# Kernel optimization log

Measured on AMD Instinct MI355X. Metric: run time of the kernel, lower is better.

The kernel has to match this reference:

```python
import jax, jax.numpy as jnp
import numpy as np

B, ES, HS, NL, NOUT, T = 16384, 64, 64, 3, 2, 128


def setup_inputs() -> dict:
    key = jax.random.key(0)
    ks = jax.random.split(key, 9)
    k = 1.0 / np.sqrt(HS)
    u = lambda kk, shape: jax.random.uniform(kk, shape, jnp.float32, -k, k)
    return {
        "agentFutureTrajEnc": jax.random.normal(ks[0], (B, ES), jnp.float32),
        "emb_w": u(ks[1], (ES, ES)),
        "emb_b": u(ks[2], (ES,)),
        "w_ih": u(ks[3], (NL, 3 * HS, ES)),
        "w_hh": u(ks[4], (NL, 3 * HS, HS)),
        "b_ih": u(ks[5], (NL, 3 * HS)),
        "b_hh": u(ks[6], (NL, 3 * HS)),
        "out_w": u(ks[7], (NOUT, HS)),
        "out_b": u(ks[8], (NOUT,)),
        "target_length": T,
        "batch_size": B,
    }


def _gru_cell(x, h, Wi, Wh, bi, bh):
    # PyTorch GRU cell math: gates ordered (r, z, n)
    gi = x @ Wi.T + bi            # (B, 3*hs)
    gh = h @ Wh.T + bh            # (B, 3*hs)
    ir, iz, inn = jnp.split(gi, 3, axis=-1)
    hr, hz, hn = jnp.split(gh, 3, axis=-1)
    r = jax.nn.sigmoid(ir + hr)
    z = jax.nn.sigmoid(iz + hz)
    n = jnp.tanh(inn + r * hn)
    return (1.0 - z) * n + z * h


def reference(agentFutureTrajEnc, emb_w, emb_b, w_ih, w_hh, b_ih, b_hh, out_w, out_b,
              target_length, batch_size):
    nl = w_ih.shape[0]
    # hidden initialized by repeating the encoding across layers: (nl, B, hs)
    h0 = jnp.broadcast_to(agentFutureTrajEnc[None], (nl,) + agentFutureTrajEnc.shape)

    def step(carry, _):
        x, h = carry                      # x: (B, es), h: (nl, B, hs)
        inp = x @ emb_w.T + emb_b         # embedding Linear(es->es)
        new_h = []
        for l in range(nl):               # small fixed layer loop
            hl = _gru_cell(inp, h[l], w_ih[l], w_hh[l], b_ih[l], b_hh[l])
            new_h.append(hl)
            inp = hl
        h = jnp.stack(new_h)              # (nl, B, hs)
        out = inp @ out_w.T + out_b       # (B, nout)
        return (h[-1], h), out            # next input is top-layer hidden

    _, outs = jax.lax.scan(step, (agentFutureTrajEnc, h0), None, length=target_length)
    return jnp.transpose(outs, (1, 0, 2))  # (B, T, nout)
```

## Files before the change

kernel.cpp:

```cpp
#include <hip/hip_runtime.h>


#define ESZ   64
#define HSZ   64
#define NLAY  3
#define TLEN  128
#define NOUTC 2
#define TILE  16
#define TILES 4
#define LDW   72
#define TB    (TILE*LDW)
#define L2E   1.44269504f

typedef _Float16 half8 __attribute__((ext_vector_type(8)));
typedef _Float16 half4 __attribute__((ext_vector_type(4)));
typedef float    floatx4 __attribute__((ext_vector_type(4)));

#define MFMA(a, b, c) __builtin_amdgcn_mfma_f32_16x16x32_f16((a), (b), (c), 0, 0, 0)

__global__ __launch_bounds__(1024, 4) void gru_pipe(
    const float* __restrict__ enc,
    const float* __restrict__ emb_w,
    const float* __restrict__ emb_b,
    const float* __restrict__ w_ih,
    const float* __restrict__ w_hh,
    const float* __restrict__ b_ih,
    const float* __restrict__ b_hh,
    const float* __restrict__ out_w,
    const float* __restrict__ out_b,
    float* __restrict__ out)
{
    __shared__ _Float16 s_emb[2 * TB];
    __shared__ _Float16 s_hl[NLAY * TILES * 2 * TB];

    const int tid   = threadIdx.x;
    const int wave  = tid >> 6, lane = tid & 63;
    const int stage = wave >> 2, g = wave & 3;
    const int q = lane >> 4, c = lane & 15;
    const int u = (g << 4) | c;
    const long wgbase = (long)blockIdx.x * (TILES * TILE);

    {
        const int row = tid >> 4;
        const int k0  = (tid & 15) << 2;
        const int j = row >> 4, rr = row & 15;
        floatx4 v = *(const floatx4*)(enc + (wgbase + row) * ESZ + k0);
        half4 h;
        #pragma unroll
        for (int x = 0; x < 4; ++x) h[x] = (_Float16)v[x];
        #pragma unroll
        for (int l = 0; l < NLAY; ++l)
            *(half4*)&s_hl[((l * TILES + j) * 2 + 1) * TB + rr * LDW + k0] = h;
    }

    auto ldw8s = [&](const float* p, float sc) {
        floatx4 a = *(const floatx4*)p, b = *(const floatx4*)(p + 4);
        half8 v;
        #pragma unroll
        for (int x = 0; x < 4; ++x) { v[x] = (_Float16)(a[x] * sc); v[4 + x] = (_Float16)(b[x] * sc); }
        return v;
    };
    half8 frag[12];
    float bias0 = 0.f, bias1 = 0.f, bias2 = 0.f, bias3 = 0.f;
    if (stage == 0) {
        frag[0] = ldw8s(emb_w + u * ESZ + q * 8, 1.f);
        frag[1] = ldw8s(emb_w + u * ESZ + 32 + q * 8, 1.f);
        const int oc = (c < NOUTC) ? c : 0;
        frag[2] = ldw8s(out_w + oc * HSZ + q * 8, 1.f);
        frag[3] = ldw8s(out_w + oc * HSZ + 32 + q * 8, 1.f);
        bias0 = emb_b[u];
        bias1 = (c < NOUTC) ? out_b[c] : 0.f;
    } else {
        const int l = stage - 1;
        const float* wi = w_ih + l * 3 * HSZ * ESZ;
        const float* wh = w_hh + l * 3 * HSZ * ESZ;
        frag[0]  = ldw8s(wi + (u) * ESZ + q * 8, -L2E);       frag[1]  = ldw8s(wi + (u) * ESZ + 32 + q * 8, -L2E);
        frag[2]  = ldw8s(wh + (u) * ESZ + q * 8, -L2E);       frag[3]  = ldw8s(wh + (u) * ESZ + 32 + q * 8, -L2E);
        frag[4]  = ldw8s(wi + (64 + u) * ESZ + q * 8, -L2E);  frag[5]  = ldw8s(wi + (64 + u) * ESZ + 32 + q * 8, -L2E);
        frag[6]  = ldw8s(wh + (64 + u) * ESZ + q * 8, -L2E);  frag[7]  = ldw8s(wh + (64 + u) * ESZ + 32 + q * 8, -L2E);
        frag[8]  = ldw8s(wi + (128 + u) * ESZ + q * 8, 2*L2E); frag[9]  = ldw8s(wi + (128 + u) * ESZ + 32 + q * 8, 2*L2E);
        frag[10] = ldw8s(wh + (128 + u) * ESZ + q * 8, 2*L2E); frag[11] = ldw8s(wh + (128 + u) * ESZ + 32 + q * 8, 2*L2E);
        const int b0 = l * 3 * HSZ;
        bias0 = -L2E * (b_ih[b0 + u] + b_hh[b0 + u]);
        bias1 = -L2E * (b_ih[b0 + 64 + u] + b_hh[b0 + 64 + u]);
        bias2 = 2.f * L2E * b_ih[b0 + 128 + u];
        bias3 = 2.f * L2E * b_hh[b0 + 128 + u];
    }

    floatx4 carr0 = {0,0,0,0}, carr1 = {0,0,0,0}, carr2 = {0,0,0,0}, carr3 = {0,0,0,0};
    if (stage >= 1) {
        floatx4 tmp[4];
        #pragma unroll
        for (int p = 0; p < 4; ++p) {
            const int jp = (p - stage) & 3;
            floatx4 hv;
            #pragma unroll
            for (int i = 0; i < 4; ++i)
                hv[i] = enc[(wgbase + jp * TILE + q * 4 + i) * ESZ + u];
            tmp[p] = hv;
        }
        carr0 = tmp[0]; carr1 = tmp[1]; carr2 = tmp[2]; carr3 = tmp[3];
    }
    const int ar = c * LDW + q * 8;
    __syncthreads();

    auto phase = [&](const int js, floatx4& carr, const int s4) {
        if (stage == 0) {
            const int j = js;
            const int t = s4;
            const _Float16* xb = &s_hl[((2 * TILES + j) * 2 + ((t + 1) & 1)) * TB];
            half8 a0 = *(const half8*)&xb[ar];
            half8 a1 = *(const half8*)&xb[ar + 32];
            if (t >= 1 && g == 0) {
                floatx4 acc = {bias1, bias1, bias1, bias1};
                acc = MFMA(a0, frag[2], acc);
                acc = MFMA(a1, frag[3], acc);
                if (c < NOUTC) {
                    #pragma unroll
                    for (int i = 0; i < 4; ++i)
                        out[((wgbase + j * TILE + q * 4 + i) * TLEN + (t - 1)) * NOUTC + c] = acc[i];
                }
            }
            if (t < TLEN) {
                floatx4 acc = {bias0, bias0, bias0, bias0};
                acc = MFMA(a0, frag[0], acc);
                acc = MFMA(a1, frag[1], acc);
                _Float16* eb = &s_emb[(js & 1) * TB];
                #pragma unroll
                for (int i = 0; i < 4; ++i)
                    eb[(q * 4 + i) * LDW + u] = (_Float16)acc[i];
            }
        } else {
            const int l = stage - 1;
            const int j = (js - stage) & 3;
            const int t = s4 - ((js < stage) ? 1 : 0);
            if (t >= 0 && t < TLEN) {
                const _Float16* xb = (stage == 1)
                    ? &s_emb[(((js & 1) ^ 1)) * TB]
                    : &s_hl[(((l - 1) * TILES + j) * 2 + (t & 1)) * TB];
                const _Float16* hb = &s_hl[((l * TILES + j) * 2 + ((t + 1) & 1)) * TB];
                half8 ax0 = *(const half8*)&xb[ar];
                half8 ax1 = *(const half8*)&xb[ar + 32];
                half8 ah0 = *(const half8*)&hb[ar];
                half8 ah1 = *(const half8*)&hb[ar + 32];
                floatx4 hold = carr;
                floatx4 accr  = {bias0, bias0, bias0, bias0};
                floatx4 accz  = {bias1, bias1, bias1, bias1};
                floatx4 accni = {bias2, bias2, bias2, bias2};
                floatx4 accnh = {bias3, bias3, bias3, bias3};
                accr  = MFMA(ax0, frag[0], accr);  accr  = MFMA(ax1, frag[1], accr);
                accr  = MFMA(ah0, frag[2], accr);  accr  = MFMA(ah1, frag[3], accr);
                accz  = MFMA(ax0, frag[4], accz);  accz  = MFMA(ax1, frag[5], accz);
                accz  = MFMA(ah0, frag[6], accz);  accz  = MFMA(ah1, frag[7], accz);
                accni = MFMA(ax0, frag[8], accni); accni = MFMA(ax1, frag[9], accni);
                accnh = MFMA(ah0, frag[10], accnh); accnh = MFMA(ah1, frag[11], accnh);
                _Float16* hw = &s_hl[((l * TILES + j) * 2 + (t & 1)) * TB];
                floatx4 hnew;
                #pragma unroll
                for (int i = 0; i < 4; ++i) {
                    const float r  = __builtin_amdgcn_rcpf(1.f + __builtin_amdgcn_exp2f(accr[i]));
                    const float z  = __builtin_amdgcn_rcpf(1.f + __builtin_amdgcn_exp2f(accz[i]));
                    const float a  = accni[i] + r * accnh[i];
                    const float n  = 1.f - 2.f * __builtin_amdgcn_rcpf(1.f + __builtin_amdgcn_exp2f(a));
                    const float hv = n + z * (hold[i] - n);
                    hnew[i] = hv;
                    hw[(q * 4 + i) * LDW + u] = (_Float16)hv;
                }
                carr = hnew;
            }
        }
        __syncthreads();
    };

    for (int s4 = 0; s4 <= TLEN; ++s4) {
        phase(0, carr0, s4);
        phase(1, carr1, s4);
        phase(2, carr2, s4);
        phase(3, carr3, s4);
    }
}

extern "C" void kernel_launch(void* const* d_in, const int* in_sizes, int n_in,
                              void* d_out, int out_size, void* d_ws, size_t ws_size,
                              hipStream_t stream) {
    (void)in_sizes; (void)n_in; (void)d_ws; (void)ws_size; (void)out_size;
    const int grid = 16384 / (TILES * TILE);
    gru_pipe<<<grid, 1024, 0, stream>>>(
        (const float*)d_in[0],
        (const float*)d_in[1],
        (const float*)d_in[2],
        (const float*)d_in[3],
        (const float*)d_in[4],
        (const float*)d_in[5],
        (const float*)d_in[6],
        (const float*)d_in[7],
        (const float*)d_in[8],
        (float*)d_out);
}
```

Before: 490.3 us.

## Fold embedding linear into layer-0 GRU input weights and drop embedding stage

Layer 0's input weights are precomposed with the embedding matrix and bias at kernel start, so the separate embedding pipeline stage and its shared buffer go away. The block shrinks from 16 to 12 waves, and every wave now runs the GRU. The recurrent-state loads for the next phase are prefetched from LDS before the current phase's math. The plain __syncthreads is replaced by a waitcnt-plus-s_barrier. The fused weights are built in fp32 and then rounded to fp16, which changes rounding slightly, and the prefetch relies on the custom barrier ordering LDS correctly.

```diff
diff --git a/kernel.cpp b/kernel.cpp
--- a/kernel.cpp
+++ b/kernel.cpp
@@ -13,12 +13,17 @@
 #define L2E   1.44269504f
 
 typedef _Float16 half8 __attribute__((ext_vector_type(8)));
-typedef _Float16 half4 __attribute__((ext_vector_type(4)));
 typedef float    floatx4 __attribute__((ext_vector_type(4)));
 
 #define MFMA(a, b, c) __builtin_amdgcn_mfma_f32_16x16x32_f16((a), (b), (c), 0, 0, 0)
 
-__global__ __launch_bounds__(1024, 4) void gru_pipe(
+__device__ __forceinline__ void wg_barrier() {
+    asm volatile("s_waitcnt lgkmcnt(0)" ::: "memory");
+    __builtin_amdgcn_s_barrier();
+    asm volatile("" ::: "memory");
+}
+
+__global__ __launch_bounds__(768, 3) void gru_pipe(
     const float* __restrict__ enc,
     const float* __restrict__ emb_w,
     const float* __restrict__ emb_b,
@@ -30,27 +35,27 @@
     const float* __restrict__ out_b,
     float* __restrict__ out)
 {
-    __shared__ _Float16 s_emb[2 * TB];
     __shared__ _Float16 s_hl[NLAY * TILES * 2 * TB];
 
-    const int tid   = threadIdx.x;
-    const int wave  = tid >> 6, lane = tid & 63;
-    const int stage = wave >> 2, g = wave & 3;
+    const int tid  = threadIdx.x;
+    const int wave = tid >> 6, lane = tid & 63;
+    const int l = wave >> 2, g = wave & 3;
     const int q = lane >> 4, c = lane & 15;
     const int u = (g << 4) | c;
     const long wgbase = (long)blockIdx.x * (TILES * TILE);
 
-    {
-        const int row = tid >> 4;
-        const int k0  = (tid & 15) << 2;
+    if (tid < 512) {
+        const int row = tid >> 3, k0 = (tid & 7) << 3;
         const int j = row >> 4, rr = row & 15;
-        floatx4 v = *(const floatx4*)(enc + (wgbase + row) * ESZ + k0);
-        half4 h;
-        #pragma unroll
-        for (int x = 0; x < 4; ++x) h[x] = (_Float16)v[x];
-        #pragma unroll
-        for (int l = 0; l < NLAY; ++l)
-            *(half4*)&s_hl[((l * TILES + j) * 2 + 1) * TB + rr * LDW + k0] = h;
+        const float* p = enc + (wgbase + row) * ESZ + k0;
+        floatx4 s0 = *(const floatx4*)p;
+        floatx4 s1 = *(const floatx4*)(p + 4);
+        half8 v;
+        #pragma unroll
+        for (int x = 0; x < 4; ++x) { v[x] = (_Float16)s0[x]; v[4 + x] = (_Float16)s1[x]; }
+        #pragma unroll
+        for (int ly = 0; ly < NLAY; ++ly)
+            *(half8*)&s_hl[((ly * TILES + j) * 2 + 1) * TB + rr * LDW + k0] = v;
     }
 
     auto ldw8s = [&](const float* p, float sc) {
@@ -60,39 +65,77 @@
         for (int x = 0; x < 4; ++x) { v[x] = (_Float16)(a[x] * sc); v[4 + x] = (_Float16)(b[x] * sc); }
         return v;
     };
-    half8 frag[12];
-    float bias0 = 0.f, bias1 = 0.f, bias2 = 0.f, bias3 = 0.f;
-    if (stage == 0) {
-        frag[0] = ldw8s(emb_w + u * ESZ + q * 8, 1.f);
-        frag[1] = ldw8s(emb_w + u * ESZ + 32 + q * 8, 1.f);
+    half8 fR[4], fZ[4], fNi[2], fNh[2], fO[2];
+    float bias0, bias1, bias2, bias3, outb = 0.f;
+    if (l == 0) {
+        const float* wi = w_ih;
+        const float* wh = w_hh;
+        floatx4 aR[4], aZ[4], aN[4];
+        #pragma unroll
+        for (int x = 0; x < 4; ++x) { aR[x] = {0,0,0,0}; aZ[x] = {0,0,0,0}; aN[x] = {0,0,0,0}; }
+        float bR = 0.f, bZ = 0.f, bN = 0.f;
+        for (int k4 = 0; k4 < 64; k4 += 4) {
+            floatx4 wr4 = *(const floatx4*)(wi + (u) * 64 + k4);
+            floatx4 wz4 = *(const floatx4*)(wi + (64 + u) * 64 + k4);
+            floatx4 wn4 = *(const floatx4*)(wi + (128 + u) * 64 + k4);
+            floatx4 be4 = *(const floatx4*)(emb_b + k4);
+            #pragma unroll
+            for (int kk = 0; kk < 4; ++kk) {
+                const float* er = emb_w + (k4 + kk) * 64;
+                floatx4 e0 = *(const floatx4*)(er + q * 8);
+                floatx4 e1 = *(const floatx4*)(er + q * 8 + 4);
+                floatx4 e2 = *(const floatx4*)(er + 32 + q * 8);
+                floatx4 e3 = *(const floatx4*)(er + 32 + q * 8 + 4);
+                const float wr = wr4[kk], wz = wz4[kk], wn = wn4[kk];
+                aR[0] += wr * e0; aR[1] += wr * e1; aR[2] += wr * e2; aR[3] += wr * e3;
+                aZ[0] += wz * e0; aZ[1] += wz * e1; aZ[2] += wz * e2; aZ[3] += wz * e3;
+                aN[0] += wn * e0; aN[1] += wn * e1; aN[2] += wn * e2; aN[3] += wn * e3;
+                bR += wr * be4[kk]; bZ += wz * be4[kk]; bN += wn * be4[kk];
+            }
+        }
+        #pragma unroll
+        for (int x = 0; x < 4; ++x) {
+            fR[0][x] = (_Float16)(-L2E * aR[0][x]);   fR[0][4 + x] = (_Float16)(-L2E * aR[1][x]);
+            fR[1][x] = (_Float16)(-L2E * aR[2][x]);   fR[1][4 + x] = (_Float16)(-L2E * aR[3][x]);
+            fZ[0][x] = (_Float16)(-L2E * aZ[0][x]);   fZ[0][4 + x] = (_Float16)(-L2E * aZ[1][x]);
+            fZ[1][x] = (_Float16)(-L2E * aZ[2][x]);   fZ[1][4 + x] = (_Float16)(-L2E * aZ[3][x]);
+            fNi[0][x] = (_Float16)(2*L2E * aN[0][x]); fNi[0][4 + x] = (_Float16)(2*L2E * aN[1][x]);
+            fNi[1][x] = (_Float16)(2*L2E * aN[2][x]); fNi[1][4 + x] = (_Float16)(2*L2E * aN[3][x]);
+        }
+        fR[2]  = ldw8s(wh + (u) * 64 + q * 8, -L2E);        fR[3]  = ldw8s(wh + (u) * 64 + 32 + q * 8, -L2E);
+        fZ[2]  = ldw8s(wh + (64 + u) * 64 + q * 8, -L2E);   fZ[3]  = ldw8s(wh + (64 + u) * 64 + 32 + q * 8, -L2E);
+        fNh[0] = ldw8s(wh + (128 + u) * 64 + q * 8, 2*L2E); fNh[1] = ldw8s(wh + (128 + u) * 64 + 32 + q * 8, 2*L2E);
+        bias0 = -L2E * (bR + b_ih[u] + b_hh[u]);
+        bias1 = -L2E * (bZ + b_ih[64 + u] + b_hh[64 + u]);
+        bias2 = 2.f * L2E * (bN + b_ih[128 + u]);
+        bias3 = 2.f * L2E * b_hh[128 + u];
         const int oc = (c < NOUTC) ? c : 0;
-        frag[2] = ldw8s(out_w + oc * HSZ + q * 8, 1.f);
-        frag[3] = ldw8s(out_w + oc * HSZ + 32 + q * 8, 1.f);
-        bias0 = emb_b[u];
-        bias1 = (c < NOUTC) ? out_b[c] : 0.f;
+        fO[0] = ldw8s(out_w + oc * 64 + q * 8, 1.f);
+        fO[1] = ldw8s(out_w + oc * 64 + 32 + q * 8, 1.f);
+        outb = (c < NOUTC) ? out_b[c] : 0.f;
     } else {
-        const int l = stage - 1;
         const float* wi = w_ih + l * 3 * HSZ * ESZ;
         const float* wh = w_hh + l * 3 * HSZ * ESZ;
-        frag[0]  = ldw8s(wi + (u) * ESZ + q * 8, -L2E);       frag[1]  = ldw8s(wi + (u) * ESZ + 32 + q * 8, -L2E);
-        frag[2]  = ldw8s(wh + (u) * ESZ + q * 8, -L2E);       frag[3]  = ldw8s(wh + (u) * ESZ + 32 + q * 8, -L2E);
-        frag[4]  = ldw8s(wi + (64 + u) * ESZ + q * 8, -L2E);  frag[5]  = ldw8s(wi + (64 + u) * ESZ + 32 + q * 8, -L2E);
-        frag[6]  = ldw8s(wh + (64 + u) * ESZ + q * 8, -L2E);  frag[7]  = ldw8s(wh + (64 + u) * ESZ + 32 + q * 8, -L2E);
-        frag[8]  = ldw8s(wi + (128 + u) * ESZ + q * 8, 2*L2E); frag[9]  = ldw8s(wi + (128 + u) * ESZ + 32 + q * 8, 2*L2E);
-        frag[10] = ldw8s(wh + (128 + u) * ESZ + q * 8, 2*L2E); frag[11] = ldw8s(wh + (128 + u) * ESZ + 32 + q * 8, 2*L2E);
+        fR[0]  = ldw8s(wi + (u) * 64 + q * 8, -L2E);        fR[1]  = ldw8s(wi + (u) * 64 + 32 + q * 8, -L2E);
+        fR[2]  = ldw8s(wh + (u) * 64 + q * 8, -L2E);        fR[3]  = ldw8s(wh + (u) * 64 + 32 + q * 8, -L2E);
+        fZ[0]  = ldw8s(wi + (64 + u) * 64 + q * 8, -L2E);   fZ[1]  = ldw8s(wi + (64 + u) * 64 + 32 + q * 8, -L2E);
+        fZ[2]  = ldw8s(wh + (64 + u) * 64 + q * 8, -L2E);   fZ[3]  = ldw8s(wh + (64 + u) * 64 + 32 + q * 8, -L2E);
+        fNi[0] = ldw8s(wi + (128 + u) * 64 + q * 8, 2*L2E); fNi[1] = ldw8s(wi + (128 + u) * 64 + 32 + q * 8, 2*L2E);
+        fNh[0] = ldw8s(wh + (128 + u) * 64 + q * 8, 2*L2E); fNh[1] = ldw8s(wh + (128 + u) * 64 + 32 + q * 8, 2*L2E);
         const int b0 = l * 3 * HSZ;
         bias0 = -L2E * (b_ih[b0 + u] + b_hh[b0 + u]);
         bias1 = -L2E * (b_ih[b0 + 64 + u] + b_hh[b0 + 64 + u]);
         bias2 = 2.f * L2E * b_ih[b0 + 128 + u];
         bias3 = 2.f * L2E * b_hh[b0 + 128 + u];
-    }
-
-    floatx4 carr0 = {0,0,0,0}, carr1 = {0,0,0,0}, carr2 = {0,0,0,0}, carr3 = {0,0,0,0};
-    if (stage >= 1) {
+        fO[0] = fO[1] = half8{};
+    }
+
+    floatx4 carr0, carr1, carr2, carr3;
+    {
         floatx4 tmp[4];
         #pragma unroll
         for (int p = 0; p < 4; ++p) {
-            const int jp = (p - stage) & 3;
+            const int jp = (p - l) & 3;
             floatx4 hv;
             #pragma unroll
             for (int i = 0; i < 4; ++i)
@@ -104,72 +147,87 @@
     const int ar = c * LDW + q * 8;
     __syncthreads();
 
+    auto gru = [&](half8 ax0, half8 ax1, half8 ah0, half8 ah1, floatx4& carr, _Float16* hw) {
+        floatx4 accr  = {bias0, bias0, bias0, bias0};
+        floatx4 accz  = {bias1, bias1, bias1, bias1};
+        floatx4 accni = {bias2, bias2, bias2, bias2};
+        floatx4 accnh = {bias3, bias3, bias3, bias3};
+        accr  = MFMA(ah0, fR[2], accr);   accr  = MFMA(ah1, fR[3], accr);
+        accz  = MFMA(ah0, fZ[2], accz);   accz  = MFMA(ah1, fZ[3], accz);
+        accnh = MFMA(ah0, fNh[0], accnh); accnh = MFMA(ah1, fNh[1], accnh);
+        accr  = MFMA(ax0, fR[0], accr);   accr  = MFMA(ax1, fR[1], accr);
+        accz  = MFMA(ax0, fZ[0], accz);   accz  = MFMA(ax1, fZ[1], accz);
+        accni = MFMA(ax0, fNi[0], accni); accni = MFMA(ax1, fNi[1], accni);
+        const floatx4 hold = carr;
+        floatx4 hnew;
+        #pragma unroll
+        for (int i = 0; i < 4; ++i) {
+            const float r  = __builtin_amdgcn_rcpf(1.f + __builtin_amdgcn_exp2f(accr[i]));
+            const float z  = __builtin_amdgcn_rcpf(1.f + __builtin_amdgcn_exp2f(accz[i]));
+            const float a  = accni[i] + r * accnh[i];
+            const float n  = 1.f - 2.f * __builtin_amdgcn_rcpf(1.f + __builtin_amdgcn_exp2f(a));
+            const float hv = n + z * (hold[i] - n);
+            hnew[i] = hv;
+            hw[(q * 4 + i) * LDW + u] = (_Float16)hv;
+        }
+        carr = hnew;
+    };
+
+    half8 ah0p, ah1p, ax0p{}, ax1p{};
+    {
+        const int jn = (0 - l) & 3;
+        const int tn = (l > 0) ? -1 : 0;
+        const _Float16* hb = &s_hl[((l * TILES + jn) * 2 + ((tn + 1) & 1)) * TB];
+        ah0p = *(const half8*)&hb[ar];
+        ah1p = *(const half8*)&hb[ar + 32];
+        if (l == 0) {
+            const _Float16* xb = &s_hl[((2 * TILES + jn) * 2 + ((tn + 1) & 1)) * TB];
+            ax0p = *(const half8*)&xb[ar];
+            ax1p = *(const half8*)&xb[ar + 32];
+        }
+    }
+
     auto phase = [&](const int js, floatx4& carr, const int s4) {
-        if (stage == 0) {
-            const int j = js;
-            const int t = s4;
-            const _Float16* xb = &s_hl[((2 * TILES + j) * 2 + ((t + 1) & 1)) * TB];
-            half8 a0 = *(const half8*)&xb[ar];
-            half8 a1 = *(const half8*)&xb[ar + 32];
+        const int j = (js - l) & 3;
+        const int t = s4 - ((js < l) ? 1 : 0);
+        const half8 ah0 = ah0p, ah1 = ah1p, ax0 = ax0p, ax1 = ax1p;
+        {
+            const int jsn = (js + 1) & 3;
+            const int s4n = s4 + ((js == 3) ? 1 : 0);
+            const int jn  = (jsn - l) & 3;
+            const int tn  = s4n - ((jsn < l) ? 1 : 0);
+            const int par = (tn + 1) & 1;
+            const _Float16* hb = &s_hl[((l * TILES + jn) * 2 + par) * TB];
+            ah0p = *(const half8*)&hb[ar];
+            ah1p = *(const half8*)&hb[ar + 32];
+            if (l == 0) {
+                const _Float16* xb = &s_hl[((2 * TILES + jn) * 2 + par) * TB];
+                ax0p = *(const half8*)&xb[ar];
+                ax1p = *(const half8*)&xb[ar + 32];
+            }
+        }
+        if (l == 0) {
             if (t >= 1 && g == 0) {
-                floatx4 acc = {bias1, bias1, bias1, bias1};
-                acc = MFMA(a0, frag[2], acc);
-                acc = MFMA(a1, frag[3], acc);
+                floatx4 acc = {outb, outb, outb, outb};
+                acc = MFMA(ax0, fO[0], acc);
+                acc = MFMA(ax1, fO[1], acc);
                 if (c < NOUTC) {
                     #pragma unroll
                     for (int i = 0; i < 4; ++i)
                         out[((wgbase + j * TILE + q * 4 + i) * TLEN + (t - 1)) * NOUTC + c] = acc[i];
                 }
             }
-            if (t < TLEN) {
-                floatx4 acc = {bias0, bias0, bias0, bias0};
-                acc = MFMA(a0, frag[0], acc);
-                acc = MFMA(a1, frag[1], acc);
-                _Float16* eb = &s_emb[(js & 1) * TB];
-                #pragma unroll
-                for (int i = 0; i < 4; ++i)
-                    eb[(q * 4 + i) * LDW + u] = (_Float16)acc[i];
-            }
+            if (t < TLEN)
+                gru(ax0, ax1, ah0, ah1, carr, &s_hl[((0 * TILES + j) * 2 + (t & 1)) * TB]);
         } else {
-            const int l = stage - 1;
-            const int j = (js - stage) & 3;
-            const int t = s4 - ((js < stage) ? 1 : 0);
             if (t >= 0 && t < TLEN) {
-                const _Float16* xb = (stage == 1)
-                    ? &s_emb[(((js & 1) ^ 1)) * TB]
-                    : &s_hl[(((l - 1) * TILES + j) * 2 + (t & 1)) * TB];
-                const _Float16* hb = &s_hl[((l * TILES + j) * 2 + ((t + 1) & 1)) * TB];
-                half8 ax0 = *(const half8*)&xb[ar];
-                half8 ax1 = *(const half8*)&xb[ar + 32];
-                half8 ah0 = *(const half8*)&hb[ar];
-                half8 ah1 = *(const half8*)&hb[ar + 32];
-                floatx4 hold = carr;
-                floatx4 accr  = {bias0, bias0, bias0, bias0};
-                floatx4 accz  = {bias1, bias1, bias1, bias1};
-                floatx4 accni = {bias2, bias2, bias2, bias2};
-                floatx4 accnh = {bias3, bias3, bias3, bias3};
-                accr  = MFMA(ax0, frag[0], accr);  accr  = MFMA(ax1, frag[1], accr);
-                accr  = MFMA(ah0, frag[2], accr);  accr  = MFMA(ah1, frag[3], accr);
-                accz  = MFMA(ax0, frag[4], accz);  accz  = MFMA(ax1, frag[5], accz);
-                accz  = MFMA(ah0, frag[6], accz);  accz  = MFMA(ah1, frag[7], accz);
-                accni = MFMA(ax0, frag[8], accni); accni = MFMA(ax1, frag[9], accni);
-                accnh = MFMA(ah0, frag[10], accnh); accnh = MFMA(ah1, frag[11], accnh);
-                _Float16* hw = &s_hl[((l * TILES + j) * 2 + (t & 1)) * TB];
-                floatx4 hnew;
-                #pragma unroll
-                for (int i = 0; i < 4; ++i) {
-                    const float r  = __builtin_amdgcn_rcpf(1.f + __builtin_amdgcn_exp2f(accr[i]));
-                    const float z  = __builtin_amdgcn_rcpf(1.f + __builtin_amdgcn_exp2f(accz[i]));
-                    const float a  = accni[i] + r * accnh[i];
-                    const float n  = 1.f - 2.f * __builtin_amdgcn_rcpf(1.f + __builtin_amdgcn_exp2f(a));
-                    const float hv = n + z * (hold[i] - n);
-                    hnew[i] = hv;
-                    hw[(q * 4 + i) * LDW + u] = (_Float16)hv;
-                }
-                carr = hnew;
-            }
-        }
-        __syncthreads();
+                const _Float16* xb = &s_hl[(((l - 1) * TILES + j) * 2 + (t & 1)) * TB];
+                half8 bx0 = *(const half8*)&xb[ar];
+                half8 bx1 = *(const half8*)&xb[ar + 32];
+                gru(bx0, bx1, ah0, ah1, carr, &s_hl[((l * TILES + j) * 2 + (t & 1)) * TB]);
+            }
+        }
+        wg_barrier();
     };
 
     for (int s4 = 0; s4 <= TLEN; ++s4) {
@@ -185,7 +243,7 @@
                               hipStream_t stream) {
     (void)in_sizes; (void)n_in; (void)d_ws; (void)ws_size; (void)out_size;
     const int grid = 16384 / (TILES * TILE);
-    gru_pipe<<<grid, 1024, 0, stream>>>(
+    gru_pipe<<<grid, 768, 0, stream>>>(
         (const float*)d_in[0],
         (const float*)d_in[1],
         (const float*)d_in[2],
```

Result: no change. 490.2 us (-0.0%).
